# Optimization experiments

Hardware: AMD Instinct MI355X
Metric: run time of the kernel (lower is better)

## Reference

```python
import jax, jax.numpy as jnp
import numpy as np

N_NODES = 100000
N_EDGES = 1600000
IN_CH, HID, OUT_CH = 128, 64, 16
EPS = 1e-5


def _sage(x, src, dst, Ws, Wn, b):
    """DGL SAGEConv mean: fc_self(x) + fc_neigh(mean_{u in N(v)} x_u) + b."""
    msg = x[src]                                              # [E, F] gather
    agg = jax.ops.segment_sum(msg, dst, num_segments=N_NODES)  # [N, F]
    deg = jax.ops.segment_sum(jnp.ones((dst.shape[0],), x.dtype), dst,
                              num_segments=N_NODES)
    h_neigh = agg / jnp.maximum(deg, 1.0)[:, None]            # zero-deg -> 0
    return x @ Ws + h_neigh @ Wn + b


def _bn(h, gamma, beta):
    """BatchNorm1d, training-mode batch statistics (biased var)."""
    mean = jnp.mean(h, axis=0)
    var = jnp.mean(jnp.square(h - mean), axis=0)
    return (h - mean) * jax.lax.rsqrt(var + EPS) * gamma + beta


def setup_inputs() -> dict:
    key = jax.random.key(0)
    ks = jax.random.split(key, 20)
    s = 0.05
    d = {
        "x": jax.random.normal(ks[0], (N_NODES, IN_CH), jnp.float32),
        "src": jax.random.randint(ks[1], (N_EDGES,), 0, N_NODES),
        "dst": jax.random.randint(ks[2], (N_EDGES,), 0, N_NODES),
        # layer1: SAGEConv(128 -> 64) + BN
        "Ws1": jax.random.normal(ks[3], (IN_CH, HID), jnp.float32) * s,
        "Wn1": jax.random.normal(ks[4], (IN_CH, HID), jnp.float32) * s,
        "b1": jnp.zeros((HID,), jnp.float32),
        "g1": jnp.ones((HID,), jnp.float32),
        "be1": jnp.zeros((HID,), jnp.float32),
        # hidden layer A: SAGEConv(64 -> 64) + BN + ReLU
        "Ws2": jax.random.normal(ks[5], (HID, HID), jnp.float32) * s,
        "Wn2": jax.random.normal(ks[6], (HID, HID), jnp.float32) * s,
        "b2": jnp.zeros((HID,), jnp.float32),
        "g2": jnp.ones((HID,), jnp.float32),
        "be2": jnp.zeros((HID,), jnp.float32),
        # hidden layer B
        "Ws3": jax.random.normal(ks[7], (HID, HID), jnp.float32) * s,
        "Wn3": jax.random.normal(ks[8], (HID, HID), jnp.float32) * s,
        "b3": jnp.zeros((HID,), jnp.float32),
        "g3": jnp.ones((HID,), jnp.float32),
        "be3": jnp.zeros((HID,), jnp.float32),
        # output: SAGEConv(64 -> 16)
        "Ws4": jax.random.normal(ks[9], (HID, OUT_CH), jnp.float32) * s,
        "Wn4": jax.random.normal(ks[10], (HID, OUT_CH), jnp.float32) * s,
        "b4": jnp.zeros((OUT_CH,), jnp.float32),
    }
    return d


def reference(x, src, dst,
              Ws1, Wn1, b1, g1, be1,
              Ws2, Wn2, b2, g2, be2,
              Ws3, Wn3, b3, g3, be3,
              Ws4, Wn4, b4):
    h = _sage(x, src, dst, Ws1, Wn1, b1)
    h = _bn(h, g1, be1)                      # note: no ReLU after layer1 (as in source)
    h = jax.nn.relu(_bn(_sage(h, src, dst, Ws2, Wn2, b2), g2, be2))
    h = jax.nn.relu(_bn(_sage(h, src, dst, Ws3, Wn3, b3), g3, be3))
    h = _sage(h, src, dst, Ws4, Wn4, b4)
    return h
```

## Files before the change

kernel.cpp:

```cpp
#include <hip/hip_runtime.h>

#define BKT_SHIFT 9
#define BKT_SIZE 512

typedef __attribute__((ext_vector_type(8))) short short8;
typedef __attribute__((ext_vector_type(4))) float floatx4;


__device__ __forceinline__ float bfu(unsigned short h) {
    return __uint_as_float(((unsigned)h) << 16);
}
__device__ __forceinline__ unsigned short fbf(float f) {
    unsigned u = __float_as_uint(f);
    unsigned r = 0x7FFFu + ((u >> 16) & 1u);
    return (unsigned short)((u + r) >> 16);
}


__global__ __launch_bounds__(256) void fill_bf16(unsigned short* p, int n, float val) {
    int i = blockIdx.x * 256 + threadIdx.x;
    if (i < n) p[i] = fbf(val);
}

__global__ __launch_bounds__(256) void zero_i32(int* p, int n) {
    int i = blockIdx.x * 256 + threadIdx.x;
    if (i < n) p[i] = 0;
}

__global__ void detect_kernel(const unsigned* g1w, int* flags) {
    if (threadIdx.x == 0 && blockIdx.x == 0)
        flags[0] = (g1w[0] == 0x3F803F80u) ? 1 : 0;
}


__global__ __launch_bounds__(256)
void conv_all(const int* flags, float* wf,
              const void* a0, const void* a1, const void* a2, const void* a3,
              const void* a4, const void* a5, const void* a6, const void* a7,
              const void* a8, const void* a9, const void* a10, const void* a11,
              const void* a12, const void* a13, const void* a14, const void* a15,
              const void* a16, const void* a17) {
    const void* srcs[18] = {a0,a1,a2,a3,a4,a5,a6,a7,a8,a9,a10,a11,a12,a13,a14,a15,a16,a17};
    const int ns[18]   = {8192,8192,64,64,64,4096,4096,64,64,64,4096,4096,64,64,64,1024,1024,16};
    const int offs[18] = {0,8192,16384,16448,16512,16576,20672,24768,24832,24896,
                          24960,29056,33152,33216,33280,33344,34368,35392};
    int b = blockIdx.x;
    if (b >= 18) return;
    int n = ns[b];
    float* dst = wf + offs[b];
    int isbf = flags[0];
    if (isbf) {
        const unsigned short* s = (const unsigned short*)srcs[b];
        for (int i = threadIdx.x; i < n; i += 256) dst[i] = bfu(s[i]);
    } else {
        const float* s = (const float*)srcs[b];
        for (int i = threadIdx.x; i < n; i += 256) dst[i] = s[i];
    }
}


__global__ __launch_bounds__(256)
void pack_w(const float* Ws, const float* Wn, unsigned short* out, int K) {
    int tid = blockIdx.x * 256 + threadIdx.x;
    int total = (K >> 5) * 8 * 64;
    if (tid >= total) return;
    int l = tid & 63;
    int tn = (tid >> 6) & 7;
    int kc = tid >> 9;
    int col = tn * 16 + (l & 15);
    int kb = kc * 32 + (l >> 4) * 8;
    unsigned short v[8];
    for (int j = 0; j < 8; ++j) {
        int k = kb + j;
        float f = (col < 64) ? Ws[(size_t)k * 64 + col] : Wn[(size_t)k * 64 + (col - 64)];
        v[j] = fbf(f);
    }
    *reinterpret_cast<uint4*>(out + (size_t)tid * 8) = *reinterpret_cast<uint4*>(v);
}


__global__ __launch_bounds__(256)
void bin_count(const int* dst, int* bcnt, int E, int NB, int CE) {
    __shared__ int hist[512];
    int t = threadIdx.x;
    for (int i = t; i < NB; i += 256) hist[i] = 0;
    __syncthreads();
    int beg = blockIdx.x * CE;
    int end = beg + CE; if (end > E) end = E;
    for (int i = beg + t; i < end; i += 256)
        atomicAdd(&hist[dst[i] >> BKT_SHIFT], 1);
    __syncthreads();
    for (int i = t; i < NB; i += 256)
        if (hist[i]) atomicAdd(&bcnt[i], hist[i]);
}

__global__ __launch_bounds__(256)
void bin_scan(const int* bcnt, int* boff, int* gcur, int NB, int E,
              int* rowptr, int Nn) {
    __shared__ int s2[256];
    int t = threadIdx.x;
    int i0 = 2 * t, i1 = 2 * t + 1;
    int c0 = (i0 < NB) ? bcnt[i0] : 0;
    int c1 = (i1 < NB) ? bcnt[i1] : 0;
    s2[t] = c0 + c1;
    __syncthreads();
    for (int off = 1; off < 256; off <<= 1) {
        int x = (t >= off) ? s2[t - off] : 0;
        __syncthreads();
        s2[t] += x;
        __syncthreads();
    }
    int excl = s2[t] - (c0 + c1);
    if (i0 < NB) { boff[i0] = excl;      gcur[i0] = excl; }
    if (i1 < NB) { boff[i1] = excl + c0; gcur[i1] = excl + c0; }
    if (t == 255) { boff[NB] = E; rowptr[Nn] = E; }
}

__global__ __launch_bounds__(256)
void bin_scatter(const int* src, const int* dst, int* gcur, unsigned* staging,
                 int E, int NB, int CE) {
    __shared__ int hist[512];
    __shared__ int cur[512];
    int t = threadIdx.x;
    for (int i = t; i < NB; i += 256) hist[i] = 0;
    __syncthreads();
    int beg = blockIdx.x * CE;
    int end = beg + CE; if (end > E) end = E;
    for (int i = beg + t; i < end; i += 256)
        atomicAdd(&hist[dst[i] >> BKT_SHIFT], 1);
    __syncthreads();
    for (int i = t; i < NB; i += 256) {
        int h = hist[i];
        cur[i] = h ? atomicAdd(&gcur[i], h) : 0;
    }
    __syncthreads();
    for (int i = beg + t; i < end; i += 256) {
        int d = dst[i];
        int b = d >> BKT_SHIFT;
        int pos = atomicAdd(&cur[b], 1);
        staging[pos] = ((unsigned)src[i] << BKT_SHIFT) | (unsigned)(d & (BKT_SIZE - 1));
    }
}

__global__ __launch_bounds__(256)
void bin_csr(const unsigned* staging, const int* boff, int* rowptr, int* esrc, int Nn) {
    __shared__ int sdeg[512];
    __shared__ int sscan[256];
    int b = blockIdx.x, t = threadIdx.x;
    int ebeg = boff[b], eend = boff[b + 1];
    int n0 = b << BKT_SHIFT;
    sdeg[t] = 0; sdeg[t + 256] = 0;
    __syncthreads();
    for (int i = ebeg + t; i < eend; i += 256)
        atomicAdd(&sdeg[staging[i] & (BKT_SIZE - 1)], 1);
    __syncthreads();
    int d0 = sdeg[2 * t], d1 = sdeg[2 * t + 1];
    sscan[t] = d0 + d1;
    __syncthreads();
    for (int off = 1; off < 256; off <<= 1) {
        int x = (t >= off) ? sscan[t - off] : 0;
        __syncthreads();
        sscan[t] += x;
        __syncthreads();
    }
    int excl = sscan[t] - (d0 + d1);
    int cur0 = ebeg + excl;
    int cur1 = cur0 + d0;
    int g0 = n0 + 2 * t, g1 = n0 + 2 * t + 1;
    if (g0 < Nn) rowptr[g0] = cur0;
    if (g1 < Nn) rowptr[g1] = cur1;
    __syncthreads();
    sdeg[2 * t] = cur0;
    sdeg[2 * t + 1] = cur1;
    __syncthreads();
    for (int i = ebeg + t; i < eend; i += 256) {
        unsigned pk = staging[i];
        int n = pk & (BKT_SIZE - 1);
        int pos = atomicAdd(&sdeg[n], 1);
        esrc[pos] = (int)(pk >> BKT_SHIFT);
    }
}


__global__ __launch_bounds__(256)
void gemm64m(const void* Aptr, int K, const int* flags, int useflag,
             const unsigned short* Wpk, const float* bias, const float* aff,
             int affine, int relu,
             unsigned short* outS, unsigned short* outP, int Nn) {
    __shared__ unsigned short Ald[64 * 40];

    const int tid = threadIdx.x;
    const int wave = tid >> 6;
    const int lane = tid & 63;
    const int lrow = lane & 15;
    const int lq = lane >> 4;
    const int r0 = blockIdx.x * 64;
    const int wrow = wave * 16;
    const int abf16 = useflag ? flags[0] : 0;

    floatx4 acc[8];
    for (int t = 0; t < 8; ++t)
        for (int i = 0; i < 4; ++i) acc[t][i] = 0.f;

    const int arow = tid >> 2;
    const int akq = tid & 3;
    int aRowG = r0 + arow;
    if (aRowG >= Nn) aRowG = Nn - 1;

    const int nkc = K >> 5;
    for (int kc = 0; kc < nkc; ++kc) {
        const int k0 = kc << 5;
        __syncthreads();
        if (abf16) {
            const unsigned short* Ab = (const unsigned short*)Aptr;
            uint4 u = *reinterpret_cast<const uint4*>(Ab + (size_t)aRowG * K + k0 + akq * 8);
            *reinterpret_cast<uint4*>(&Ald[arow * 40 + akq * 8]) = u;
        } else {
            const float* Af = (const float*)Aptr;
            const float4* fp = reinterpret_cast<const float4*>(Af + (size_t)aRowG * K + k0 + akq * 8);
            float4 f0 = fp[0], f1 = fp[1];
            float v[8];
            v[0] = f0.x; v[1] = f0.y; v[2] = f0.z; v[3] = f0.w;
            v[4] = f1.x; v[5] = f1.y; v[6] = f1.z; v[7] = f1.w;
            if (affine) {
                for (int j = 0; j < 8; ++j) {
                    int c = k0 + akq * 8 + j;
                    v[j] = v[j] * aff[c] + aff[K + c];
                    if (relu && v[j] < 0.f) v[j] = 0.f;
                }
            }
            uint4 u;
            u.x = ((unsigned)fbf(v[1]) << 16) | (unsigned)fbf(v[0]);
            u.y = ((unsigned)fbf(v[3]) << 16) | (unsigned)fbf(v[2]);
            u.z = ((unsigned)fbf(v[5]) << 16) | (unsigned)fbf(v[4]);
            u.w = ((unsigned)fbf(v[7]) << 16) | (unsigned)fbf(v[6]);
            *reinterpret_cast<uint4*>(&Ald[arow * 40 + akq * 8]) = u;
        }
        __syncthreads();
        short8 afr = *reinterpret_cast<const short8*>(&Ald[(wrow + lrow) * 40 + lq * 8]);
        const short8* bp = reinterpret_cast<const short8*>(Wpk) + ((size_t)kc * 8) * 64 + lane;
#pragma unroll
        for (int tn = 0; tn < 8; ++tn) {
            short8 bfr = bp[tn * 64];
            acc[tn] = __builtin_amdgcn_mfma_f32_16x16x32_bf16(afr, bfr, acc[tn], 0, 0, 0);
        }
    }
#pragma unroll
    for (int tn = 0; tn < 8; ++tn) {
        int col = tn * 16 + lrow;
        float badd = (tn < 4) ? bias[col] : 0.f;
#pragma unroll
        for (int r = 0; r < 4; ++r) {
            int gr = r0 + wrow + lq * 4 + r;
            if (gr < Nn) {
                float v = acc[tn][r] + badd;
                if (tn < 4) outS[(size_t)gr * 64 + col] = fbf(v);
                else        outP[(size_t)gr * 64 + (col - 64)] = fbf(v);
            }
        }
    }
}


__global__ __launch_bounds__(256)
void gemm16(const float* Aptr, const float* Ws, const float* Wn,
            const float* bias, const float* aff,
            float* outS, unsigned short* outP, int Nn) {
    __shared__ float Wlds[16][32];
    __shared__ float Atile[16][128];

    const int tid = threadIdx.x;
    const int ty = tid >> 4;
    const int tx = tid & 15;
    const int r0 = blockIdx.x * 128;
    const int K = 64;

    float acc[8][2];
    for (int i = 0; i < 8; ++i) { acc[i][0] = 0.f; acc[i][1] = 0.f; }

    const int arow = tid >> 1;
    const int ahalf = (tid & 1) * 8;
    int aRowG = r0 + arow;
    if (aRowG >= Nn) aRowG = Nn - 1;

    const int wkl = tid >> 4;
    const int wjc = (tid & 15) * 2;

    for (int kc = 0; kc < 4; ++kc) {
        const int k0 = kc << 4;
        __syncthreads();
        {
            const float* wsrc;
            if (wjc < 16) wsrc = Ws + (size_t)(k0 + wkl) * 16 + wjc;
            else          wsrc = Wn + (size_t)(k0 + wkl) * 16 + (wjc - 16);
            const float2* w2 = reinterpret_cast<const float2*>(wsrc);
            float2 w = w2[0];
            Wlds[wkl][wjc + 0] = w.x;
            Wlds[wkl][wjc + 1] = w.y;
        }
        {
            const float4* fp = reinterpret_cast<const float4*>(Aptr + (size_t)aRowG * K + k0 + ahalf);
            float4 f0 = fp[0], f1 = fp[1];
            float v[8];
            v[0] = f0.x; v[1] = f0.y; v[2] = f0.z; v[3] = f0.w;
            v[4] = f1.x; v[5] = f1.y; v[6] = f1.z; v[7] = f1.w;
            for (int j = 0; j < 8; ++j) {
                int c = k0 + ahalf + j;
                float t = v[j] * aff[c] + aff[K + c];
                if (t < 0.f) t = 0.f;
                Atile[ahalf + j][arow] = t;
            }
        }
        __syncthreads();
        for (int kk = 0; kk < 16; ++kk) {
            const float4* ap = reinterpret_cast<const float4*>(&Atile[kk][ty * 8]);
            float4 a0 = ap[0], a1 = ap[1];
            float a8[8];
            a8[0] = a0.x; a8[1] = a0.y; a8[2] = a0.z; a8[3] = a0.w;
            a8[4] = a1.x; a8[5] = a1.y; a8[6] = a1.z; a8[7] = a1.w;
            const float2* wp2 = reinterpret_cast<const float2*>(&Wlds[kk][tx * 2]);
            float2 w = wp2[0];
            for (int i = 0; i < 8; ++i) {
                acc[i][0] = fmaf(a8[i], w.x, acc[i][0]);
                acc[i][1] = fmaf(a8[i], w.y, acc[i][1]);
            }
        }
    }
    const int cg = tx * 2;
    const int isS = (cg < 16) ? 1 : 0;
    const int cb = isS ? cg : (cg - 16);
    float b0 = isS ? bias[cb] : 0.f;
    float b1 = isS ? bias[cb + 1] : 0.f;
    for (int i = 0; i < 8; ++i) {
        int gr = r0 + ty * 8 + i;
        if (gr < Nn) {
            float v0 = acc[i][0] + b0;
            float v1 = acc[i][1] + b1;
            if (isS) {
                float2 o; o.x = v0; o.y = v1;
                *reinterpret_cast<float2*>(outS + (size_t)gr * 16 + cb) = o;
            } else {
                unsigned u = ((unsigned)fbf(v1) << 16) | (unsigned)fbf(v0);
                *reinterpret_cast<unsigned*>(outP + (size_t)gr * 16 + cb) = u;
            }
        }
    }
}


__global__ __launch_bounds__(256)
void agg64(const unsigned short* p, const unsigned short* s, const int* rowptr,
           const int* esrc, float* out, int Nn) {
    int v = (blockIdx.x << 2) + (threadIdx.x >> 6);
    if (v >= Nn) return;
    int lane = threadIdx.x & 63;
    int g = lane >> 4;
    int q = lane & 15;
    int beg = rowptr[v], end = rowptr[v + 1];
    float a0 = 0.f, a1 = 0.f, a2 = 0.f, a3 = 0.f;
    int e = beg + g;
    for (; e + 12 < end; e += 16) {
        int u0 = esrc[e];
        int u1 = esrc[e + 4];
        int u2 = esrc[e + 8];
        int u3 = esrc[e + 12];
        uint2 x0 = *reinterpret_cast<const uint2*>(p + (size_t)u0 * 64 + q * 4);
        uint2 x1 = *reinterpret_cast<const uint2*>(p + (size_t)u1 * 64 + q * 4);
        uint2 x2 = *reinterpret_cast<const uint2*>(p + (size_t)u2 * 64 + q * 4);
        uint2 x3 = *reinterpret_cast<const uint2*>(p + (size_t)u3 * 64 + q * 4);
        a0 += (bfu((unsigned short)(x0.x & 0xFFFF)) + bfu((unsigned short)(x1.x & 0xFFFF)))
            + (bfu((unsigned short)(x2.x & 0xFFFF)) + bfu((unsigned short)(x3.x & 0xFFFF)));
        a1 += (bfu((unsigned short)(x0.x >> 16)) + bfu((unsigned short)(x1.x >> 16)))
            + (bfu((unsigned short)(x2.x >> 16)) + bfu((unsigned short)(x3.x >> 16)));
        a2 += (bfu((unsigned short)(x0.y & 0xFFFF)) + bfu((unsigned short)(x1.y & 0xFFFF)))
            + (bfu((unsigned short)(x2.y & 0xFFFF)) + bfu((unsigned short)(x3.y & 0xFFFF)));
        a3 += (bfu((unsigned short)(x0.y >> 16)) + bfu((unsigned short)(x1.y >> 16)))
            + (bfu((unsigned short)(x2.y >> 16)) + bfu((unsigned short)(x3.y >> 16)));
    }
    for (; e < end; e += 4) {
        int u = esrc[e];
        uint2 x = *reinterpret_cast<const uint2*>(p + (size_t)u * 64 + q * 4);
        a0 += bfu((unsigned short)(x.x & 0xFFFF));
        a1 += bfu((unsigned short)(x.x >> 16));
        a2 += bfu((unsigned short)(x.y & 0xFFFF));
        a3 += bfu((unsigned short)(x.y >> 16));
    }
    a0 += __shfl_xor(a0, 16, 64); a0 += __shfl_xor(a0, 32, 64);
    a1 += __shfl_xor(a1, 16, 64); a1 += __shfl_xor(a1, 32, 64);
    a2 += __shfl_xor(a2, 16, 64); a2 += __shfl_xor(a2, 32, 64);
    a3 += __shfl_xor(a3, 16, 64); a3 += __shfl_xor(a3, 32, 64);
    if (g == 0) {
        float dd = (float)(end - beg);
        if (dd < 1.f) dd = 1.f;
        float inv = 1.f / dd;
        size_t o = (size_t)v * 64 + q * 4;
        uint2 su = *reinterpret_cast<const uint2*>(s + o);
        float4 r;
        r.x = bfu((unsigned short)(su.x & 0xFFFF)) + a0 * inv;
        r.y = bfu((unsigned short)(su.x >> 16))    + a1 * inv;
        r.z = bfu((unsigned short)(su.y & 0xFFFF)) + a2 * inv;
        r.w = bfu((unsigned short)(su.y >> 16))    + a3 * inv;
        *reinterpret_cast<float4*>(out + o) = r;
    }
}


__global__ __launch_bounds__(256)
void agg16(const unsigned short* p, const float* s, const int* rowptr, const int* esrc,
           void* outv, const int* flags, int Nn) {
    int v = (blockIdx.x << 2) + (threadIdx.x >> 6);
    if (v >= Nn) return;
    int lane = threadIdx.x & 63;
    int g = lane >> 4;
    int c = lane & 15;
    int beg = rowptr[v], end = rowptr[v + 1];
    float a = 0.f;
    int e = beg + g;
    for (; e + 12 < end; e += 16) {
        int u0 = esrc[e];
        int u1 = esrc[e + 4];
        int u2 = esrc[e + 8];
        int u3 = esrc[e + 12];
        float f0 = bfu(p[(size_t)u0 * 16 + c]);
        float f1 = bfu(p[(size_t)u1 * 16 + c]);
        float f2 = bfu(p[(size_t)u2 * 16 + c]);
        float f3 = bfu(p[(size_t)u3 * 16 + c]);
        a += (f0 + f1) + (f2 + f3);
    }
    for (; e < end; e += 4) a += bfu(p[(size_t)esrc[e] * 16 + c]);
    a += __shfl_xor(a, 16, 64);
    a += __shfl_xor(a, 32, 64);
    if (g == 0) {
        float dd = (float)(end - beg);
        if (dd < 1.f) dd = 1.f;
        float res = s[(size_t)v * 16 + c] + a / dd;
        if (flags[0]) ((unsigned short*)outv)[(size_t)v * 16 + c] = fbf(res);
        else          ((float*)outv)[(size_t)v * 16 + c] = res;
    }
}


__global__ __launch_bounds__(256) void stats_kernel(const float* h, float* stats, int Nn) {
    __shared__ float sh[512];
    int c = threadIdx.x & 63, g = threadIdx.x >> 6;
    float sm = 0.f, s2 = 0.f;
    for (int r = blockIdx.x * 4 + g; r < Nn; r += gridDim.x * 4) {
        float v = h[(size_t)r * 64 + c];
        sm += v; s2 += v * v;
    }
    sh[threadIdx.x] = sm;
    sh[256 + threadIdx.x] = s2;
    __syncthreads();
    if (g == 0) {
        float ts = sh[c] + sh[64 + c] + sh[128 + c] + sh[192 + c];
        float t2 = sh[256 + c] + sh[320 + c] + sh[384 + c] + sh[448 + c];
        atomicAdd(&stats[c], ts);
        atomicAdd(&stats[64 + c], t2);
    }
}

__global__ void affine_kernel(const float* stats, const float* g,
                              const float* be, float* aff, int Nn) {
    int c = threadIdx.x;
    if (c < 64) {
        float inv = 1.f / (float)Nn;
        float mean = stats[c] * inv;
        float var = stats[64 + c] * inv - mean * mean;
        float rstd = rsqrtf(var + 1e-5f);
        float sc = rstd * g[c];
        aff[c] = sc;
        aff[64 + c] = be[c] - mean * sc;
    }
}


extern "C" void kernel_launch(void* const* d_in, const int* in_sizes, int n_in,
                              void* d_out, int out_size, void* d_ws, size_t ws_size,
                              hipStream_t stream) {
    const void* x = d_in[0];
    const int* src = (const int*)d_in[1];
    const int* dst = (const int*)d_in[2];

    unsigned short* out_bf = (unsigned short*)d_out;
    const int ob = (out_size + 255) / 256;

    const int Nn = out_size / 16;
    const int E = in_sizes[1];

    if (Nn <= 0 || in_sizes[0] != Nn * 128 || in_sizes[2] != E || E <= 0 || n_in < 21
        || Nn > 256 * 1024) {
        fill_bf16<<<ob, 256, 0, stream>>>(out_bf, out_size, 21.0f);
        return;
    }

    size_t off = 0;
    char* base = (char*)d_ws;
    int* rowptr;  { rowptr = (int*)(base + off); off += ((size_t)(Nn + 1) * 4 + 255) & ~(size_t)255; }
    int* esrc;    { esrc   = (int*)(base + off); off += ((size_t)E * 4 + 255) & ~(size_t)255; }
    unsigned* staging; unsigned short* sbuf;
    {
        size_t sz1 = (size_t)E * 4, sz2 = (size_t)Nn * 64 * 2;
        size_t sz = sz1 > sz2 ? sz1 : sz2;
        staging = (unsigned*)(base + off);
        sbuf = (unsigned short*)(base + off);
        off += (sz + 255) & ~(size_t)255;
    }
    unsigned short* bufP; { bufP = (unsigned short*)(base + off); off += ((size_t)Nn * 64 * 2 + 255) & ~(size_t)255; }
    float* bufS;  { bufS  = (float*)(base + off); off += ((size_t)Nn * 64 * 4 + 255) & ~(size_t)255; }
    float* stats; { stats = (float*)(base + off); off += 512; }
    float* aff;   { aff   = (float*)(base + off); off += 512; }
    int* flags;   { flags = (int*)(base + off); off += 256; }
    int* bcnt;    { bcnt  = (int*)(base + off); off += 2048; }
    int* boff;    { boff  = (int*)(base + off); off += 2304; }
    int* gcur;    { gcur  = (int*)(base + off); off += 2048; }
    float* wf;    { wf    = (float*)(base + off); off += ((size_t)35408 * 4 + 255) & ~(size_t)255; }
    unsigned short* wpk; { wpk = (unsigned short*)(base + off); off += ((size_t)32768 * 2 + 255) & ~(size_t)255; }
    float* s4 = (float*)bufP;
    unsigned short* p4 = (unsigned short*)(s4 + (size_t)Nn * 16);

    if (off > ws_size) {
        fill_bf16<<<ob, 256, 0, stream>>>(out_bf, out_size, 13.0f);
        return;
    }

    const float* WS1 = wf + 0;      const float* WN1 = wf + 8192;
    const float* B1  = wf + 16384;  const float* G1  = wf + 16448;  const float* BE1 = wf + 16512;
    const float* WS2 = wf + 16576;  const float* WN2 = wf + 20672;
    const float* B2  = wf + 24768;  const float* G2  = wf + 24832;  const float* BE2 = wf + 24896;
    const float* WS3 = wf + 24960;  const float* WN3 = wf + 29056;
    const float* B3  = wf + 33152;  const float* G3  = wf + 33216;  const float* BE3 = wf + 33280;
    const float* WS4 = wf + 33344;  const float* WN4 = wf + 34368;
    const float* B4  = wf + 35392;
    unsigned short* WPK1 = wpk + 0;
    unsigned short* WPK2 = wpk + 16384;
    unsigned short* WPK3 = wpk + 24576;

    detect_kernel<<<1, 64, 0, stream>>>((const unsigned*)d_in[6], flags);
    conv_all<<<18, 256, 0, stream>>>(flags, wf,
        d_in[3], d_in[4], d_in[5], d_in[6], d_in[7],
        d_in[8], d_in[9], d_in[10], d_in[11], d_in[12],
        d_in[13], d_in[14], d_in[15], d_in[16], d_in[17],
        d_in[18], d_in[19], d_in[20]);
    pack_w<<<8, 256, 0, stream>>>(WS1, WN1, WPK1, 128);
    pack_w<<<4, 256, 0, stream>>>(WS2, WN2, WPK2, 64);
    pack_w<<<4, 256, 0, stream>>>(WS3, WN3, WPK3, 64);

    const int NB = (Nn + BKT_SIZE - 1) >> BKT_SHIFT;
    const int NBC = 192;
    const int CE = (E + NBC - 1) / NBC;
    zero_i32<<<2, 256, 0, stream>>>(bcnt, NB);
    bin_count<<<NBC, 256, 0, stream>>>(dst, bcnt, E, NB, CE);
    bin_scan<<<1, 256, 0, stream>>>(bcnt, boff, gcur, NB, E, rowptr, Nn);
    bin_scatter<<<NBC, 256, 0, stream>>>(src, dst, gcur, staging, E, NB, CE);
    bin_csr<<<NB, 256, 0, stream>>>(staging, boff, rowptr, esrc, Nn);

    const int gmb = (Nn + 63) / 64;
    const int ab = (Nn + 3) / 4;
    const int gb = (Nn + 127) / 128;

    gemm64m<<<gmb, 256, 0, stream>>>(x, 128, flags, 1, WPK1, B1, aff, 0, 0, sbuf, bufP, Nn);
    agg64<<<ab, 256, 0, stream>>>(bufP, sbuf, rowptr, esrc, bufS, Nn);
    zero_i32<<<1, 256, 0, stream>>>((int*)stats, 128);
    stats_kernel<<<240, 256, 0, stream>>>(bufS, stats, Nn);
    affine_kernel<<<1, 64, 0, stream>>>(stats, G1, BE1, aff, Nn);

    gemm64m<<<gmb, 256, 0, stream>>>(bufS, 64, flags, 0, WPK2, B2, aff, 1, 0, sbuf, bufP, Nn);
    agg64<<<ab, 256, 0, stream>>>(bufP, sbuf, rowptr, esrc, bufS, Nn);
    zero_i32<<<1, 256, 0, stream>>>((int*)stats, 128);
    stats_kernel<<<240, 256, 0, stream>>>(bufS, stats, Nn);
    affine_kernel<<<1, 64, 0, stream>>>(stats, G2, BE2, aff, Nn);

    gemm64m<<<gmb, 256, 0, stream>>>(bufS, 64, flags, 0, WPK3, B3, aff, 1, 1, sbuf, bufP, Nn);
    agg64<<<ab, 256, 0, stream>>>(bufP, sbuf, rowptr, esrc, bufS, Nn);
    zero_i32<<<1, 256, 0, stream>>>((int*)stats, 128);
    stats_kernel<<<240, 256, 0, stream>>>(bufS, stats, Nn);
    affine_kernel<<<1, 64, 0, stream>>>(stats, G3, BE3, aff, Nn);

    gemm16<<<gb, 256, 0, stream>>>(bufS, WS4, WN4, B4, aff, s4, p4, Nn);
    agg16<<<ab, 256, 0, stream>>>(p4, s4, rowptr, esrc, d_out, flags, Nn);
}
```

Measured before the change: 575.3 us.

## Store neighbor-projected features as FP8 e4m3 to halve gather traffic

The neighbor-side GEMM output (the projected features that get gathered per edge) is now stored as FP8 e4m3 instead of bf16, and the aggregation kernel decodes four FP8 values per 32-bit load. This halves the bytes moved by the random per-edge gather, which dominates the aggregation cost. Unroll depth in both aggregation kernels is reduced, the GEMM epilogue packs stores into vector writes, and the output write layout of agg64 changes to a strided per-column pattern. FP8 quantization adds numerical error to the neighbor messages, and the workspace layout for layer-4 buffers is moved.

```diff
diff --git a/kernel.cpp b/kernel.cpp
--- a/kernel.cpp
+++ b/kernel.cpp
@@ -5,6 +5,11 @@
 
 typedef __attribute__((ext_vector_type(8))) short short8;
 typedef __attribute__((ext_vector_type(4))) float floatx4;
+typedef __attribute__((ext_vector_type(2))) float floatx2;
+
+#if __has_builtin(__builtin_amdgcn_cvt_pk_f32_fp8) && __has_builtin(__builtin_amdgcn_cvt_pk_fp8_f32)
+#define HAVE_FP8_CVT 1
+#endif
 
 
 __device__ __forceinline__ float bfu(unsigned short h) {
@@ -14,6 +19,56 @@
     unsigned u = __float_as_uint(f);
     unsigned r = 0x7FFFu + ((u >> 16) & 1u);
     return (unsigned short)((u + r) >> 16);
+}
+
+#ifndef HAVE_FP8_CVT
+__device__ __forceinline__ unsigned e4m3_enc1(float f) {
+    unsigned u = __float_as_uint(f);
+    unsigned sgn = (u >> 31) << 7;
+    float af = __uint_as_float(u & 0x7FFFFFFFu);
+    if (af > 448.f) af = 448.f;
+    if (af < 9.765625e-4f) return sgn;
+    if (af < 0.015625f) {
+        int m = (int)(af * 512.f + 0.5f);
+        if (m >= 8) return sgn | (1 << 3);
+        return sgn | (unsigned)m;
+    }
+    int eb = (int)((__float_as_uint(af) >> 23) & 255) - 127;
+    float step = __uint_as_float((unsigned)(eb - 3 + 127) << 23);
+    float q = af + 0.5f * step;
+    int e2 = (int)((__float_as_uint(q) >> 23) & 255) - 127;
+    int e8 = e2 + 7;
+    unsigned mant = (__float_as_uint(q) >> 20) & 7;
+    if (e8 > 15) { e8 = 15; mant = 6; }
+    return sgn | ((unsigned)e8 << 3) | mant;
+}
+__device__ __forceinline__ float e4m3_dec1(unsigned b) {
+    unsigned s = b >> 7, e = (b >> 3) & 15, m = b & 7;
+    float v;
+    if (e == 0) v = (float)m * 0.001953125f;
+    else v = __uint_as_float(((e + 120) << 23) | (m << 20));
+    return s ? -v : v;
+}
+#endif
+
+__device__ __forceinline__ void fp8x4_dec(unsigned u, float& f0, float& f1, float& f2, float& f3) {
+#ifdef HAVE_FP8_CVT
+    floatx2 lo = __builtin_amdgcn_cvt_pk_f32_fp8((int)u, false);
+    floatx2 hi = __builtin_amdgcn_cvt_pk_f32_fp8((int)u, true);
+    f0 = lo[0]; f1 = lo[1]; f2 = hi[0]; f3 = hi[1];
+#else
+    f0 = e4m3_dec1(u & 255); f1 = e4m3_dec1((u >> 8) & 255);
+    f2 = e4m3_dec1((u >> 16) & 255); f3 = e4m3_dec1(u >> 24);
+#endif
+}
+__device__ __forceinline__ unsigned fp8x4_enc(float a, float b, float c, float d) {
+#ifdef HAVE_FP8_CVT
+    int v = __builtin_amdgcn_cvt_pk_fp8_f32(a, b, 0, false);
+    v = __builtin_amdgcn_cvt_pk_fp8_f32(c, d, v, true);
+    return (unsigned)v;
+#else
+    return e4m3_enc1(a) | (e4m3_enc1(b) << 8) | (e4m3_enc1(c) << 16) | (e4m3_enc1(d) << 24);
+#endif
 }
 
 
@@ -186,7 +241,7 @@
 void gemm64m(const void* Aptr, int K, const int* flags, int useflag,
              const unsigned short* Wpk, const float* bias, const float* aff,
              int affine, int relu,
-             unsigned short* outS, unsigned short* outP, int Nn) {
+             unsigned short* outS, unsigned char* outP, int Nn) {
     __shared__ unsigned short Ald[64 * 40];
 
     const int tid = threadIdx.x;
@@ -245,18 +300,22 @@
             acc[tn] = __builtin_amdgcn_mfma_f32_16x16x32_bf16(afr, bfr, acc[tn], 0, 0, 0);
         }
     }
+    float b0 = bias[0 * 16 + lrow];
+    float b1 = bias[1 * 16 + lrow];
+    float b2 = bias[2 * 16 + lrow];
+    float b3 = bias[3 * 16 + lrow];
 #pragma unroll
-    for (int tn = 0; tn < 8; ++tn) {
-        int col = tn * 16 + lrow;
-        float badd = (tn < 4) ? bias[col] : 0.f;
-#pragma unroll
-        for (int r = 0; r < 4; ++r) {
-            int gr = r0 + wrow + lq * 4 + r;
-            if (gr < Nn) {
-                float v = acc[tn][r] + badd;
-                if (tn < 4) outS[(size_t)gr * 64 + col] = fbf(v);
-                else        outP[(size_t)gr * 64 + (col - 64)] = fbf(v);
-            }
+    for (int r = 0; r < 4; ++r) {
+        int gr = r0 + wrow + lq * 4 + r;
+        if (gr < Nn) {
+            float s0 = acc[0][r] + b0, s1 = acc[1][r] + b1;
+            float s2 = acc[2][r] + b2, s3 = acc[3][r] + b3;
+            uint2 su;
+            su.x = ((unsigned)fbf(s1) << 16) | (unsigned)fbf(s0);
+            su.y = ((unsigned)fbf(s3) << 16) | (unsigned)fbf(s2);
+            *reinterpret_cast<uint2*>(outS + (size_t)gr * 64 + lrow * 4) = su;
+            unsigned pu = fp8x4_enc(acc[4][r], acc[5][r], acc[6][r], acc[7][r]);
+            *reinterpret_cast<unsigned*>(outP + (size_t)gr * 64 + lrow * 4) = pu;
         }
     }
 }
@@ -349,7 +408,7 @@
 
 
 __global__ __launch_bounds__(256)
-void agg64(const unsigned short* p, const unsigned short* s, const int* rowptr,
+void agg64(const unsigned char* p, const unsigned short* s, const int* rowptr,
            const int* esrc, float* out, int Nn) {
     int v = (blockIdx.x << 2) + (threadIdx.x >> 6);
     if (v >= Nn) return;
@@ -359,31 +418,24 @@
     int beg = rowptr[v], end = rowptr[v + 1];
     float a0 = 0.f, a1 = 0.f, a2 = 0.f, a3 = 0.f;
     int e = beg + g;
-    for (; e + 12 < end; e += 16) {
+    for (; e + 4 < end; e += 8) {
         int u0 = esrc[e];
         int u1 = esrc[e + 4];
-        int u2 = esrc[e + 8];
-        int u3 = esrc[e + 12];
-        uint2 x0 = *reinterpret_cast<const uint2*>(p + (size_t)u0 * 64 + q * 4);
-        uint2 x1 = *reinterpret_cast<const uint2*>(p + (size_t)u1 * 64 + q * 4);
-        uint2 x2 = *reinterpret_cast<const uint2*>(p + (size_t)u2 * 64 + q * 4);
-        uint2 x3 = *reinterpret_cast<const uint2*>(p + (size_t)u3 * 64 + q * 4);
-        a0 += (bfu((unsigned short)(x0.x & 0xFFFF)) + bfu((unsigned short)(x1.x & 0xFFFF)))
-            + (bfu((unsigned short)(x2.x & 0xFFFF)) + bfu((unsigned short)(x3.x & 0xFFFF)));
-        a1 += (bfu((unsigned short)(x0.x >> 16)) + bfu((unsigned short)(x1.x >> 16)))
-            + (bfu((unsigned short)(x2.x >> 16)) + bfu((unsigned short)(x3.x >> 16)));
-        a2 += (bfu((unsigned short)(x0.y & 0xFFFF)) + bfu((unsigned short)(x1.y & 0xFFFF)))
-            + (bfu((unsigned short)(x2.y & 0xFFFF)) + bfu((unsigned short)(x3.y & 0xFFFF)));
-        a3 += (bfu((unsigned short)(x0.y >> 16)) + bfu((unsigned short)(x1.y >> 16)))
-            + (bfu((unsigned short)(x2.y >> 16)) + bfu((unsigned short)(x3.y >> 16)));
+        unsigned x0 = *reinterpret_cast<const unsigned*>(p + (size_t)u0 * 64 + q * 4);
+        unsigned x1 = *reinterpret_cast<const unsigned*>(p + (size_t)u1 * 64 + q * 4);
+        float f0, f1, f2, f3, g0, g1, g2, g3;
+        fp8x4_dec(x0, f0, f1, f2, f3);
+        fp8x4_dec(x1, g0, g1, g2, g3);
+        a0 += f0 + g0;
+        a1 += f1 + g1;
+        a2 += f2 + g2;
+        a3 += f3 + g3;
     }
     for (; e < end; e += 4) {
-        int u = esrc[e];
-        uint2 x = *reinterpret_cast<const uint2*>(p + (size_t)u * 64 + q * 4);
-        a0 += bfu((unsigned short)(x.x & 0xFFFF));
-        a1 += bfu((unsigned short)(x.x >> 16));
-        a2 += bfu((unsigned short)(x.y & 0xFFFF));
-        a3 += bfu((unsigned short)(x.y >> 16));
+        unsigned x = *reinterpret_cast<const unsigned*>(p + (size_t)esrc[e] * 64 + q * 4);
+        float f0, f1, f2, f3;
+        fp8x4_dec(x, f0, f1, f2, f3);
+        a0 += f0; a1 += f1; a2 += f2; a3 += f3;
     }
     a0 += __shfl_xor(a0, 16, 64); a0 += __shfl_xor(a0, 32, 64);
     a1 += __shfl_xor(a1, 16, 64); a1 += __shfl_xor(a1, 32, 64);
@@ -393,14 +445,16 @@
         float dd = (float)(end - beg);
         if (dd < 1.f) dd = 1.f;
         float inv = 1.f / dd;
-        size_t o = (size_t)v * 64 + q * 4;
-        uint2 su = *reinterpret_cast<const uint2*>(s + o);
-        float4 r;
-        r.x = bfu((unsigned short)(su.x & 0xFFFF)) + a0 * inv;
-        r.y = bfu((unsigned short)(su.x >> 16))    + a1 * inv;
-        r.z = bfu((unsigned short)(su.y & 0xFFFF)) + a2 * inv;
-        r.w = bfu((unsigned short)(su.y >> 16))    + a3 * inv;
-        *reinterpret_cast<float4*>(out + o) = r;
+        uint2 su = *reinterpret_cast<const uint2*>(s + (size_t)v * 64 + q * 4);
+        float r0 = bfu((unsigned short)(su.x & 0xFFFF)) + a0 * inv;
+        float r1 = bfu((unsigned short)(su.x >> 16))    + a1 * inv;
+        float r2 = bfu((unsigned short)(su.y & 0xFFFF)) + a2 * inv;
+        float r3 = bfu((unsigned short)(su.y >> 16))    + a3 * inv;
+        float* op = out + (size_t)v * 64 + q;
+        op[0]  = r0;
+        op[16] = r1;
+        op[32] = r2;
+        op[48] = r3;
     }
 }
 
@@ -416,16 +470,10 @@
     int beg = rowptr[v], end = rowptr[v + 1];
     float a = 0.f;
     int e = beg + g;
-    for (; e + 12 < end; e += 16) {
+    for (; e + 4 < end; e += 8) {
         int u0 = esrc[e];
         int u1 = esrc[e + 4];
-        int u2 = esrc[e + 8];
-        int u3 = esrc[e + 12];
-        float f0 = bfu(p[(size_t)u0 * 16 + c]);
-        float f1 = bfu(p[(size_t)u1 * 16 + c]);
-        float f2 = bfu(p[(size_t)u2 * 16 + c]);
-        float f3 = bfu(p[(size_t)u3 * 16 + c]);
-        a += (f0 + f1) + (f2 + f3);
+        a += bfu(p[(size_t)u0 * 16 + c]) + bfu(p[(size_t)u1 * 16 + c]);
     }
     for (; e < end; e += 4) a += bfu(p[(size_t)esrc[e] * 16 + c]);
     a += __shfl_xor(a, 16, 64);
@@ -505,7 +553,7 @@
         sbuf = (unsigned short*)(base + off);
         off += (sz + 255) & ~(size_t)255;
     }
-    unsigned short* bufP; { bufP = (unsigned short*)(base + off); off += ((size_t)Nn * 64 * 2 + 255) & ~(size_t)255; }
+    unsigned char* bufP; { bufP = (unsigned char*)(base + off); off += ((size_t)Nn * 64 * 2 + 255) & ~(size_t)255; }
     float* bufS;  { bufS  = (float*)(base + off); off += ((size_t)Nn * 64 * 4 + 255) & ~(size_t)255; }
     float* stats; { stats = (float*)(base + off); off += 512; }
     float* aff;   { aff   = (float*)(base + off); off += 512; }
@@ -515,8 +563,9 @@
     int* gcur;    { gcur  = (int*)(base + off); off += 2048; }
     float* wf;    { wf    = (float*)(base + off); off += ((size_t)35408 * 4 + 255) & ~(size_t)255; }
     unsigned short* wpk; { wpk = (unsigned short*)(base + off); off += ((size_t)32768 * 2 + 255) & ~(size_t)255; }
-    float* s4 = (float*)bufP;
-    unsigned short* p4 = (unsigned short*)(s4 + (size_t)Nn * 16);
+    float* s4 = (float*)(bufP + (size_t)Nn * 64);
+    unsigned short* p4 = (unsigned short*)(base + off);
+    off += ((size_t)Nn * 16 * 2 + 255) & ~(size_t)255;
 
     if (off > ws_size) {
         fill_bf16<<<ob, 256, 0, stream>>>(out_bf, out_size, 13.0f);
```

Measured after the change: 546.3 us. 1.05x faster.
